# Kernel optimization log

Hardware: AMD Instinct MI355X
Metric: run time of the kernel (lower is better)

## Reference

```python
import jax, jax.numpy as jnp
import numpy as np
import math

N_NODES = 50000
N_EDGES = 400000
D = 256
H = 4
HD = D // H


def _layernorm(x, g, b, eps=1e-5):
    mu = jnp.mean(x, axis=-1, keepdims=True)
    var = jnp.mean((x - mu) ** 2, axis=-1, keepdims=True)
    return (x - mu) * jax.lax.rsqrt(var + eps) * g + b


def setup_inputs() -> dict:
    key = jax.random.key(0)
    ks = jax.random.split(key, 16)
    init = lambda k, sh: (jax.random.normal(k, sh, dtype=jnp.float32) * 0.02)
    inp = {
        "h_n": jax.random.normal(ks[0], (N_NODES, D), dtype=jnp.float32),
        "h_e": jax.random.normal(ks[1], (N_EDGES, D), dtype=jnp.float32),
        "edge_index": jax.random.randint(ks[2], (2, N_EDGES), 0, N_NODES, dtype=jnp.int64),
        "Wq_w": init(ks[3], (2 * D, D)), "Wq_b": jnp.zeros((D,), jnp.float32),
        "Wkv_w": init(ks[4], (2 * D, 2 * D)), "Wkv_b": jnp.zeros((2 * D,), jnp.float32),
        "Wo_w": init(ks[5], (D, D)), "Wo_b": jnp.zeros((D,), jnp.float32),
        "ln1_g": jnp.ones((D,), jnp.float32), "ln1_b": jnp.zeros((D,), jnp.float32),
        "ffn1_w": init(ks[6], (D, 4 * D)), "ffn1_b": jnp.zeros((4 * D,), jnp.float32),
        "ffn2_w": init(ks[7], (4 * D, D)), "ffn2_b": jnp.zeros((D,), jnp.float32),
        "ln2_g": jnp.ones((D,), jnp.float32), "ln2_b": jnp.zeros((D,), jnp.float32),
    }
    return inp


def reference(h_n, h_e, edge_index, Wq_w, Wq_b, Wkv_w, Wkv_b, Wo_w, Wo_b,
              ln1_g, ln1_b, ffn1_w, ffn1_b, ffn2_w, ffn2_b, ln2_g, ln2_b):
    num_nodes = h_n.shape[0]
    src, dst = edge_index[0], edge_index[1]

    # edge gathers
    q_input = jnp.concatenate([h_n[src], h_e], axis=-1)   # (E, 2D)
    kv_input = jnp.concatenate([h_n[dst], h_e], axis=-1)  # (E, 2D)

    Q = q_input @ Wq_w + Wq_b                             # (E, D)
    KV = kv_input @ Wkv_w + Wkv_b                         # (E, 2D)
    K, V = KV[:, :D], KV[:, D:]

    Q = Q.reshape(-1, H, HD)
    K = K.reshape(-1, H, HD)
    V = V.reshape(-1, H, HD)

    scores = jnp.sum(Q * K, axis=-1) / math.sqrt(HD)      # (E, H)

    # scatter softmax over edges grouped by src node
    m = jax.ops.segment_max(scores, src, num_segments=num_nodes)  # (N, H)
    ex = jnp.exp(scores - m[src])
    denom = jax.ops.segment_sum(ex, src, num_segments=num_nodes)  # (N, H)
    attn = ex / denom[src]                                        # (E, H)

    # scatter-sum of weighted values back to src nodes
    wv = attn[:, :, None] * V                                     # (E, H, HD)
    out = jax.ops.segment_sum(wv, src, num_segments=num_nodes)    # (N, H, HD)
    out = out.reshape(num_nodes, D)
    out = out @ Wo_w + Wo_b

    h = _layernorm(h_n + out, ln1_g, ln1_b)
    ff = jax.nn.gelu(h @ ffn1_w + ffn1_b, approximate=False) @ ffn2_w + ffn2_b
    h = _layernorm(h + ff, ln2_g, ln2_b)
    return h
```

## Files before the change

kernel.cpp:

```cpp
#include <hip/hip_runtime.h>
#include <hip/hip_bf16.h>
#include <cstdint>
#include <cstddef>


typedef __bf16 bf16;
typedef bf16 bf16x8 __attribute__((ext_vector_type(8)));
typedef bf16 bf16x4v __attribute__((ext_vector_type(4)));
typedef float f32x4 __attribute__((ext_vector_type(4)));
typedef const uint32_t __attribute__((address_space(1)))* gas_u32p;
typedef uint32_t __attribute__((address_space(3)))* las_u32p;

#define DEV static __device__ __forceinline__

static constexpr int NN = 50000;
static constexpr int NE = 400000;

DEV void async_copy16(const void* g, void* l) {
  __builtin_amdgcn_global_load_lds((gas_u32p)g, (las_u32p)l, 16, 0, 0);
}
DEV float bf2f(bf16 x) { return (float)x; }
DEV bf16  f2bf(float x) { return (bf16)x; }

template <int KT, int EPI>
__global__ __launch_bounds__(256, 2) void gemm_node(
    const bf16* __restrict__ A, int M, const bf16* __restrict__ WT,
    const float* __restrict__ bias, int Nout, float* __restrict__ outf,
    bf16* __restrict__ outb) {
  __shared__ bf16 Al[128 * 32];
  __shared__ bf16 Bl[128 * 32];
  const int tid = threadIdx.x;
  const int n0 = blockIdx.x * 128;
  const int m0 = blockIdx.y * 128;
  const bf16* ab[2];
  const bf16* bb[2];
#pragma unroll
  for (int p = 0; p < 2; ++p) {
    int c = tid + 256 * p;
    int row = c >> 2;
    int c8 = (c & 3) * 8;
    int rg = m0 + row;
    if (rg > M - 1) rg = M - 1;
    ab[p] = A + (size_t)rg * KT + c8;
    bb[p] = WT + (size_t)(n0 + row) * KT + c8;
  }
  const int wv = tid >> 6, lane = tid & 63;
  const int quad = lane >> 4, l16 = lane & 15;
  const int wrow = (wv >> 1) * 64, wcol = (wv & 1) * 64;
  f32x4 acc[4][4] = {};
  for (int k0 = 0; k0 < KT; k0 += 32) {
    if (k0) __syncthreads();
#pragma unroll
    for (int p = 0; p < 2; ++p) {
      async_copy16(ab[p] + k0, &Al[(tid + 256 * p) * 8]);
      async_copy16(bb[p] + k0, &Bl[(tid + 256 * p) * 8]);
    }
    __syncthreads();
    bf16x8 af[4], bfr[4];
#pragma unroll
    for (int t = 0; t < 4; ++t)
      af[t] = *(const bf16x8*)&Al[(wrow + t * 16 + l16) * 32 + quad * 8];
#pragma unroll
    for (int t = 0; t < 4; ++t)
      bfr[t] = *(const bf16x8*)&Bl[(wcol + t * 16 + l16) * 32 + quad * 8];
#pragma unroll
    for (int mt = 0; mt < 4; ++mt)
#pragma unroll
      for (int nt = 0; nt < 4; ++nt)
        acc[mt][nt] = __builtin_amdgcn_mfma_f32_16x16x32_bf16(
            af[mt], bfr[nt], acc[mt][nt], 0, 0, 0);
  }
#pragma unroll
  for (int nt = 0; nt < 4; ++nt) {
    int col = n0 + wcol + nt * 16 + l16;
    float bv = bias ? bias[col] : 0.f;
#pragma unroll
    for (int mt = 0; mt < 4; ++mt)
#pragma unroll
      for (int r = 0; r < 4; ++r) {
        int row = m0 + wrow + mt * 16 + quad * 4 + r;
        if (row < M) {
          float v = acc[mt][nt][r] + bv;
          if (EPI == 0)
            outf[(size_t)row * Nout + col] = v;
          else if (EPI == 1)
            outb[(size_t)row * Nout + col] =
                f2bf(0.5f * v * (1.f + erff(v * 0.70710678118654752f)));
          else
            outb[(size_t)row * Nout + col] = f2bf(v);
        }
      }
  }
}

__global__ __launch_bounds__(256, 2) void gemm_eeq(
    const bf16* __restrict__ he, const bf16* __restrict__ WT,
    const float* __restrict__ bias, const int* __restrict__ src,
    const float* __restrict__ ENf, bf16* __restrict__ Qout) {
  __shared__ bf16 Al[128 * 32];
  __shared__ bf16 Bl[128 * 32];
  const int tid = threadIdx.x;
  const int n0 = blockIdx.x * 128;
  const int m0 = blockIdx.y * 128;
  const bf16* ab[2];
  const bf16* bb[2];
#pragma unroll
  for (int p = 0; p < 2; ++p) {
    int c = tid + 256 * p;
    int row = c >> 2;
    int c8 = (c & 3) * 8;
    ab[p] = he + (size_t)(m0 + row) * 256 + c8;
    bb[p] = WT + (size_t)(n0 + row) * 256 + c8;
  }
  const int wv = tid >> 6, lane = tid & 63;
  const int quad = lane >> 4, l16 = lane & 15;
  const int wrow = (wv >> 1) * 64, wcol = (wv & 1) * 64;
  f32x4 acc[4][4] = {};
  for (int k0 = 0; k0 < 256; k0 += 32) {
    if (k0) __syncthreads();
#pragma unroll
    for (int p = 0; p < 2; ++p) {
      async_copy16(ab[p] + k0, &Al[(tid + 256 * p) * 8]);
      async_copy16(bb[p] + k0, &Bl[(tid + 256 * p) * 8]);
    }
    __syncthreads();
    bf16x8 af[4], bfr[4];
#pragma unroll
    for (int t = 0; t < 4; ++t)
      af[t] = *(const bf16x8*)&Al[(wrow + t * 16 + l16) * 32 + quad * 8];
#pragma unroll
    for (int t = 0; t < 4; ++t)
      bfr[t] = *(const bf16x8*)&Bl[(wcol + t * 16 + l16) * 32 + quad * 8];
#pragma unroll
    for (int mt = 0; mt < 4; ++mt)
#pragma unroll
      for (int nt = 0; nt < 4; ++nt)
        acc[mt][nt] = __builtin_amdgcn_mfma_f32_16x16x32_bf16(
            af[mt], bfr[nt], acc[mt][nt], 0, 0, 0);
  }
  float bv[4];
#pragma unroll
  for (int nt = 0; nt < 4; ++nt) bv[nt] = bias[n0 + wcol + nt * 16 + l16];
#pragma unroll
  for (int mt = 0; mt < 4; ++mt)
#pragma unroll
    for (int r = 0; r < 4; ++r) {
      int row = m0 + wrow + mt * 16 + quad * 4 + r;
      int s = src[row];
      const float* en = ENf + (size_t)s * 512;
#pragma unroll
      for (int nt = 0; nt < 4; ++nt) {
        int col = n0 + wcol + nt * 16 + l16;
        Qout[(size_t)row * 256 + col] = f2bf(acc[mt][nt][r] + bv[nt] + en[col]);
      }
    }
}

__global__ __launch_bounds__(256, 2) void gemm_eek(
    const bf16* __restrict__ he, const bf16* __restrict__ WT,
    const float* __restrict__ bias, const int* __restrict__ dstp,
    const float* __restrict__ ENf, const bf16* __restrict__ Qbf,
    float* __restrict__ scores) {
  __shared__ bf16 Al[128 * 32];
  __shared__ bf16 Bl[128 * 32];
  const int tid = threadIdx.x;
  const int n0 = blockIdx.x * 128;
  const int m0 = blockIdx.y * 128;
  const bf16* ab[2];
  const bf16* bb[2];
#pragma unroll
  for (int p = 0; p < 2; ++p) {
    int c = tid + 256 * p;
    int row = c >> 2;
    int c8 = (c & 3) * 8;
    ab[p] = he + (size_t)(m0 + row) * 256 + c8;
    bb[p] = WT + (size_t)(n0 + row) * 256 + c8;
  }
  const int wv = tid >> 6, lane = tid & 63;
  const int quad = lane >> 4, l16 = lane & 15;
  const int wrow = (wv >> 1) * 64, wcol = (wv & 1) * 64;
  f32x4 acc[4][4] = {};
  for (int k0 = 0; k0 < 256; k0 += 32) {
    if (k0) __syncthreads();
#pragma unroll
    for (int p = 0; p < 2; ++p) {
      async_copy16(ab[p] + k0, &Al[(tid + 256 * p) * 8]);
      async_copy16(bb[p] + k0, &Bl[(tid + 256 * p) * 8]);
    }
    __syncthreads();
    bf16x8 af[4], bfr[4];
#pragma unroll
    for (int t = 0; t < 4; ++t)
      af[t] = *(const bf16x8*)&Al[(wrow + t * 16 + l16) * 32 + quad * 8];
#pragma unroll
    for (int t = 0; t < 4; ++t)
      bfr[t] = *(const bf16x8*)&Bl[(wcol + t * 16 + l16) * 32 + quad * 8];
#pragma unroll
    for (int mt = 0; mt < 4; ++mt)
#pragma unroll
      for (int nt = 0; nt < 4; ++nt)
        acc[mt][nt] = __builtin_amdgcn_mfma_f32_16x16x32_bf16(
            af[mt], bfr[nt], acc[mt][nt], 0, 0, 0);
  }
  float bv[4];
#pragma unroll
  for (int nt = 0; nt < 4; ++nt) bv[nt] = bias[n0 + wcol + nt * 16 + l16];
  const int head = (n0 + wcol) >> 6;
#pragma unroll
  for (int mt = 0; mt < 4; ++mt)
#pragma unroll
    for (int r = 0; r < 4; ++r) {
      int row = m0 + wrow + mt * 16 + quad * 4 + r;
      int d = dstp[row];
      const float* en = ENf + (size_t)d * 512 + 256;
      const bf16* qr = Qbf + (size_t)row * 256;
      float part = 0.f;
#pragma unroll
      for (int nt = 0; nt < 4; ++nt) {
        int col = n0 + wcol + nt * 16 + l16;
        float kv = acc[mt][nt][r] + bv[nt] + en[col];
        part += kv * bf2f(qr[col]);
      }
      part += __shfl_xor(part, 1);
      part += __shfl_xor(part, 2);
      part += __shfl_xor(part, 4);
      part += __shfl_xor(part, 8);
      if (l16 == 0) scores[(size_t)row * 4 + head] = part * 0.125f;
    }
}

__global__ __launch_bounds__(256) void cast_bf16(const float* __restrict__ in,
                                                 bf16* __restrict__ out, int n) {
  int i = (blockIdx.x * 256 + threadIdx.x) * 4;
  if (i < n) {
    float4 v = *(const float4*)(in + i);
    bf16x4v o = {f2bf(v.x), f2bf(v.y), f2bf(v.z), f2bf(v.w)};
    *(bf16x4v*)(out + i) = o;
  }
}

__global__ __launch_bounds__(256) void transpose_cast(
    const float* __restrict__ W, bf16* __restrict__ WT, int K, int N) {
  int i = blockIdx.x * 256 + threadIdx.x;
  if (i < K * N) {
    int k = i / N, n = i - k * N;
    WT[(size_t)n * K + k] = f2bf(W[i]);
  }
}

__global__ __launch_bounds__(256) void build_wnet(
    const float* __restrict__ Wq, const float* __restrict__ Wkv,
    bf16* __restrict__ WnT, bf16* __restrict__ WeT) {
  int n = blockIdx.x, k = threadIdx.x;
  float vn, ve;
  if (n < 256) {
    vn = Wq[(size_t)k * 256 + n];
    ve = Wq[(size_t)(256 + k) * 256 + n];
  } else {
    vn = Wkv[(size_t)k * 512 + (n - 256)];
    ve = Wkv[(size_t)(256 + k) * 512 + (n - 256)];
  }
  WnT[(size_t)n * 256 + k] = f2bf(vn);
  WeT[(size_t)n * 256 + k] = f2bf(ve);
}

__global__ __launch_bounds__(256) void build_wcomb(
    const float* __restrict__ Wkv, const float* __restrict__ Wkv_b,
    const float* __restrict__ Wo, const float* __restrict__ Wo_b,
    bf16* __restrict__ WcombT, float* __restrict__ bias_vo) {
  int j = blockIdx.x, t = threadIdx.x;
  __shared__ float wo[256];
  wo[t] = Wo[(size_t)t * 256 + j];
  __syncthreads();
#pragma unroll
  for (int p = 0; p < 8; ++p) {
    int idx = p * 256 + t;
    int h = idx >> 9, i = idx & 511;
    const float* wrow = Wkv + (size_t)i * 512 + 256 + h * 64;
    const float* wob = wo + h * 64;
    float s = 0.f;
#pragma unroll 8
    for (int m = 0; m < 64; ++m) s += wrow[m] * wob[m];
    WcombT[(size_t)j * 2048 + idx] = f2bf(s);
  }
  float bs = Wkv_b[256 + t] * wo[t];
#pragma unroll
  for (int o = 32; o; o >>= 1) bs += __shfl_xor(bs, o);
  __shared__ float red[4];
  int wv = t >> 6, lane = t & 63;
  if (lane == 0) red[wv] = bs;
  __syncthreads();
  if (t == 0) bias_vo[j] = red[0] + red[1] + red[2] + red[3] + Wo_b[j];
}

__global__ __launch_bounds__(256) void count_deg(const int* __restrict__ src,
                                                 int* __restrict__ deg, int nE) {
  int e = blockIdx.x * 256 + threadIdx.x;
  if (e < nE) atomicAdd(&deg[src[e]], 1);
}

__global__ __launch_bounds__(256) void scan_offs(const int* __restrict__ deg,
                                                 int* __restrict__ offs,
                                                 int* __restrict__ cursor,
                                                 int nN) {
  __shared__ int part[256];
  int tid = threadIdx.x;
  int per = (nN + 255) >> 8;
  int lo = tid * per, hi = lo + per;
  if (hi > nN) hi = nN;
  int sm = 0;
  for (int i = lo; i < hi; ++i) sm += deg[i];
  part[tid] = sm;
  __syncthreads();
  if (tid == 0) {
    int run = 0;
    for (int i = 0; i < 256; ++i) {
      int v = part[i];
      part[i] = run;
      run += v;
    }
  }
  __syncthreads();
  int run = part[tid];
  for (int i = lo; i < hi; ++i) {
    offs[i] = run;
    cursor[i] = run;
    run += deg[i];
  }
  if (tid == 255) offs[nN] = run;
}

__global__ __launch_bounds__(256) void scatter_edges(const int* __restrict__ src,
                                                     int* __restrict__ cursor,
                                                     int* __restrict__ eperm,
                                                     int nE) {
  int e = blockIdx.x * 256 + threadIdx.x;
  if (e < nE) {
    int p = atomicAdd(&cursor[src[e]], 1);
    eperm[p] = e;
  }
}

__global__ __launch_bounds__(256) void aggregate(
    const int* __restrict__ offs, const int* __restrict__ eperm,
    const int* __restrict__ dstp, const float* __restrict__ scores,
    const bf16* __restrict__ hn, const bf16* __restrict__ he,
    bf16* __restrict__ aggH) {
  int n = blockIdx.x;
  int s = offs[n];
  int deg = offs[n + 1] - s;
  int tid = threadIdx.x, wv = tid >> 6, lane = tid & 63;
  __shared__ float mdl[4], dnl[4];
  float mx = -3.4e38f;
  for (int i = lane; i < deg; i += 64) {
    int e = eperm[s + i];
    mx = fmaxf(mx, scores[(size_t)e * 4 + wv]);
  }
#pragma unroll
  for (int o = 32; o; o >>= 1) mx = fmaxf(mx, __shfl_xor(mx, o));
  float sm = 0.f;
  for (int i = lane; i < deg; i += 64) {
    int e = eperm[s + i];
    sm += expf(scores[(size_t)e * 4 + wv] - mx);
  }
#pragma unroll
  for (int o = 32; o; o >>= 1) sm += __shfl_xor(sm, o);
  if (lane == 0) {
    mdl[wv] = mx;
    dnl[wv] = sm;
  }
  __syncthreads();
  float m[4], rd[4];
#pragma unroll
  for (int h = 0; h < 4; ++h) {
    m[h] = mdl[h];
    rd[h] = dnl[h] > 0.f ? 1.f / dnl[h] : 0.f;
  }
  float accn[4] = {}, acce[4] = {};
  for (int i = 0; i < deg; ++i) {
    int e = eperm[s + i];
    int d = dstp[e];
    f32x4 sc = *(const f32x4*)(scores + (size_t)e * 4);
    float w[4];
#pragma unroll
    for (int h = 0; h < 4; ++h) w[h] = expf(sc[h] - m[h]) * rd[h];
    float xn = bf2f(hn[(size_t)d * 256 + tid]);
    float xe = bf2f(he[(size_t)e * 256 + tid]);
#pragma unroll
    for (int h = 0; h < 4; ++h) {
      accn[h] += w[h] * xn;
      acce[h] += w[h] * xe;
    }
  }
  bf16* out = aggH + (size_t)n * 2048;
#pragma unroll
  for (int h = 0; h < 4; ++h) {
    out[h * 512 + tid] = f2bf(accn[h]);
    out[h * 512 + 256 + tid] = f2bf(acce[h]);
  }
}

__global__ __launch_bounds__(256) void ln_kernel(
    const float* __restrict__ x1, const float* __restrict__ x2,
    const float* __restrict__ g, const float* __restrict__ b,
    float* __restrict__ outf, bf16* __restrict__ outb) {
  int n = blockIdx.x, tid = threadIdx.x;
  float x = x1[(size_t)n * 256 + tid] + x2[(size_t)n * 256 + tid];
  float s = x, s2 = x * x;
#pragma unroll
  for (int o = 32; o; o >>= 1) {
    s += __shfl_xor(s, o);
    s2 += __shfl_xor(s2, o);
  }
  __shared__ float ls[4], ls2[4];
  int wv = tid >> 6, lane = tid & 63;
  if (lane == 0) {
    ls[wv] = s;
    ls2[wv] = s2;
  }
  __syncthreads();
  s = ls[0] + ls[1] + ls[2] + ls[3];
  s2 = ls2[0] + ls2[1] + ls2[2] + ls2[3];
  float mu = s * (1.f / 256.f);
  float var = s2 * (1.f / 256.f) - mu * mu;
  float y = (x - mu) * rsqrtf(var + 1e-5f) * g[tid] + b[tid];
  if (outf) outf[(size_t)n * 256 + tid] = y;
  if (outb) outb[(size_t)n * 256 + tid] = f2bf(y);
}

static constexpr size_t OFF_HN    = 0;
static constexpr size_t OFF_HE    = 25600000;
static constexpr size_t OFF_WNT   = 230400000;
static constexpr size_t OFF_WET   = 230662144;
static constexpr size_t OFF_WCT   = 230924288;
static constexpr size_t OFF_W1T   = 231972864;
static constexpr size_t OFF_W2T   = 232497152;
static constexpr size_t OFF_BVO   = 233021440;
static constexpr size_t OFF_SC    = 233022464;
static constexpr size_t OFF_DEG   = 239422464;
static constexpr size_t OFF_OFFS  = 239622464;
static constexpr size_t OFF_CUR   = 239822528;
static constexpr size_t OFF_EPERM = 240022528;
static constexpr size_t OFF_ENF   = 241622528;
static constexpr size_t OFF_Q     = 344022528;
static constexpr size_t OFF_AGGH  = OFF_Q;
static constexpr size_t OFF_TMP   = OFF_HE;
static constexpr size_t OFF_H1F   = OFF_HE + 51200000;
static constexpr size_t OFF_H1B   = OFF_HE + 102400000;
static constexpr size_t OFF_TMP2  = OFF_HE + 128000000;
static constexpr size_t OFF_FFM   = OFF_Q;

extern "C" void kernel_launch(void* const* d_in, const int* in_sizes, int n_in,
                              void* d_out, int out_size, void* d_ws,
                              size_t ws_size, hipStream_t stream) {
  const float* h_n = (const float*)d_in[0];
  const float* h_e = (const float*)d_in[1];
  const int* eidx = (const int*)d_in[2];
  const int* src = eidx;
  const int* dst = eidx + NE;
  const float* Wq_w = (const float*)d_in[3];
  const float* Wq_b = (const float*)d_in[4];
  const float* Wkv_w = (const float*)d_in[5];
  const float* Wkv_b = (const float*)d_in[6];
  const float* Wo_w = (const float*)d_in[7];
  const float* Wo_b = (const float*)d_in[8];
  const float* ln1_g = (const float*)d_in[9];
  const float* ln1_b = (const float*)d_in[10];
  const float* f1_w = (const float*)d_in[11];
  const float* f1_b = (const float*)d_in[12];
  const float* f2_w = (const float*)d_in[13];
  const float* f2_b = (const float*)d_in[14];
  const float* ln2_g = (const float*)d_in[15];
  const float* ln2_b = (const float*)d_in[16];

  uint8_t* ws = (uint8_t*)d_ws;
  bf16* hn_bf = (bf16*)(ws + OFF_HN);
  bf16* he_bf = (bf16*)(ws + OFF_HE);
  bf16* WnT = (bf16*)(ws + OFF_WNT);
  bf16* WeT = (bf16*)(ws + OFF_WET);
  bf16* WcombT = (bf16*)(ws + OFF_WCT);
  bf16* W1T = (bf16*)(ws + OFF_W1T);
  bf16* W2T = (bf16*)(ws + OFF_W2T);
  float* bias_vo = (float*)(ws + OFF_BVO);
  float* scores = (float*)(ws + OFF_SC);
  int* deg = (int*)(ws + OFF_DEG);
  int* offs = (int*)(ws + OFF_OFFS);
  int* cursor = (int*)(ws + OFF_CUR);
  int* eperm = (int*)(ws + OFF_EPERM);
  float* ENf = (float*)(ws + OFF_ENF);
  bf16* Qbf = (bf16*)(ws + OFF_Q);
  bf16* aggH = (bf16*)(ws + OFF_AGGH);
  float* tmp = (float*)(ws + OFF_TMP);
  float* h1f = (float*)(ws + OFF_H1F);
  bf16* h1b = (bf16*)(ws + OFF_H1B);
  float* tmp2 = (float*)(ws + OFF_TMP2);
  bf16* ffm = (bf16*)(ws + OFF_FFM);

  cast_bf16<<<12500, 256, 0, stream>>>(h_n, hn_bf, NN * 256);
  cast_bf16<<<100000, 256, 0, stream>>>(h_e, he_bf, NE * 256);
  build_wnet<<<512, 256, 0, stream>>>(Wq_w, Wkv_w, WnT, WeT);
  build_wcomb<<<256, 256, 0, stream>>>(Wkv_w, Wkv_b, Wo_w, Wo_b, WcombT,
                                       bias_vo);
  transpose_cast<<<1024, 256, 0, stream>>>(f1_w, W1T, 256, 1024);
  transpose_cast<<<1024, 256, 0, stream>>>(f2_w, W2T, 1024, 256);

  hipMemsetAsync(deg, 0, NN * sizeof(int), stream);
  count_deg<<<1563, 256, 0, stream>>>(src, deg, NE);
  scan_offs<<<1, 256, 0, stream>>>(deg, offs, cursor, NN);
  scatter_edges<<<1563, 256, 0, stream>>>(src, cursor, eperm, NE);

  gemm_node<256, 0><<<dim3(4, 391), 256, 0, stream>>>(hn_bf, NN, WnT, nullptr,
                                                      512, ENf, nullptr);
  gemm_eeq<<<dim3(2, 3125), 256, 0, stream>>>(he_bf, WeT, Wq_b, src, ENf, Qbf);
  gemm_eek<<<dim3(2, 3125), 256, 0, stream>>>(he_bf, WeT + 256 * 256, Wkv_b,
                                              dst, ENf, Qbf, scores);

  aggregate<<<NN, 256, 0, stream>>>(offs, eperm, dst, scores, hn_bf, he_bf,
                                    aggH);

  gemm_node<2048, 0><<<dim3(2, 391), 256, 0, stream>>>(aggH, NN, WcombT,
                                                       bias_vo, 256, tmp,
                                                       nullptr);
  ln_kernel<<<NN, 256, 0, stream>>>(h_n, tmp, ln1_g, ln1_b, h1f, h1b);

  gemm_node<256, 1><<<dim3(8, 391), 256, 0, stream>>>(h1b, NN, W1T, f1_b, 1024,
                                                      nullptr, ffm);
  gemm_node<1024, 0><<<dim3(2, 391), 256, 0, stream>>>(ffm, NN, W2T, f2_b, 256,
                                                       tmp2, nullptr);
  ln_kernel<<<NN, 256, 0, stream>>>(h1f, tmp2, ln2_g, ln2_b, (float*)d_out,
                                    nullptr);
}
```

Before: 1.896 ms.

## Fuse Q/K edge GEMMs and sort edge data by source node

Merges the separate Q and K edge GEMMs into one kernel that computes both accumulators from a shared A tile and forms attention scores directly. This removes the bf16 Q round-trip through global memory and one pass over h_e. Edge features, src and dst are permuted into src-sorted order during the bf16 cast, so the aggregate kernel reads edges contiguously instead of through eperm. The aggregate kernel also precomputes softmax weights per 64-edge chunk in shared memory. In exchange the fused GEMM holds twice the accumulators, which raises register pressure, and the cast now does a gathered read.

```diff
diff --git a/kernel.cpp b/kernel.cpp
--- a/kernel.cpp
+++ b/kernel.cpp
@@ -83,143 +83,93 @@
           float v = acc[mt][nt][r] + bv;
           if (EPI == 0)
             outf[(size_t)row * Nout + col] = v;
-          else if (EPI == 1)
+          else
             outb[(size_t)row * Nout + col] =
                 f2bf(0.5f * v * (1.f + erff(v * 0.70710678118654752f)));
-          else
-            outb[(size_t)row * Nout + col] = f2bf(v);
         }
       }
   }
 }
 
-__global__ __launch_bounds__(256, 2) void gemm_eeq(
-    const bf16* __restrict__ he, const bf16* __restrict__ WT,
-    const float* __restrict__ bias, const int* __restrict__ src,
-    const float* __restrict__ ENf, bf16* __restrict__ Qout) {
+__global__ __launch_bounds__(256, 2) void gemm_qk(
+    const bf16* __restrict__ he, const bf16* __restrict__ WTq,
+    const bf16* __restrict__ WTk, const float* __restrict__ bq,
+    const float* __restrict__ bk, const int* __restrict__ sp,
+    const int* __restrict__ dp, const float* __restrict__ ENf,
+    float* __restrict__ scores) {
   __shared__ bf16 Al[128 * 32];
-  __shared__ bf16 Bl[128 * 32];
+  __shared__ bf16 Bq[128 * 32];
+  __shared__ bf16 Bk[128 * 32];
   const int tid = threadIdx.x;
   const int n0 = blockIdx.x * 128;
   const int m0 = blockIdx.y * 128;
   const bf16* ab[2];
-  const bf16* bb[2];
+  const bf16* bqp[2];
+  const bf16* bkp[2];
 #pragma unroll
   for (int p = 0; p < 2; ++p) {
     int c = tid + 256 * p;
     int row = c >> 2;
     int c8 = (c & 3) * 8;
     ab[p] = he + (size_t)(m0 + row) * 256 + c8;
-    bb[p] = WT + (size_t)(n0 + row) * 256 + c8;
+    bqp[p] = WTq + (size_t)(n0 + row) * 256 + c8;
+    bkp[p] = WTk + (size_t)(n0 + row) * 256 + c8;
   }
   const int wv = tid >> 6, lane = tid & 63;
   const int quad = lane >> 4, l16 = lane & 15;
   const int wrow = (wv >> 1) * 64, wcol = (wv & 1) * 64;
-  f32x4 acc[4][4] = {};
+  f32x4 aq[4][4] = {};
+  f32x4 ak[4][4] = {};
   for (int k0 = 0; k0 < 256; k0 += 32) {
     if (k0) __syncthreads();
 #pragma unroll
     for (int p = 0; p < 2; ++p) {
       async_copy16(ab[p] + k0, &Al[(tid + 256 * p) * 8]);
-      async_copy16(bb[p] + k0, &Bl[(tid + 256 * p) * 8]);
+      async_copy16(bqp[p] + k0, &Bq[(tid + 256 * p) * 8]);
+      async_copy16(bkp[p] + k0, &Bk[(tid + 256 * p) * 8]);
     }
     __syncthreads();
-    bf16x8 af[4], bfr[4];
+    bf16x8 af[4];
 #pragma unroll
     for (int t = 0; t < 4; ++t)
       af[t] = *(const bf16x8*)&Al[(wrow + t * 16 + l16) * 32 + quad * 8];
 #pragma unroll
-    for (int t = 0; t < 4; ++t)
-      bfr[t] = *(const bf16x8*)&Bl[(wcol + t * 16 + l16) * 32 + quad * 8];
-#pragma unroll
-    for (int mt = 0; mt < 4; ++mt)
-#pragma unroll
-      for (int nt = 0; nt < 4; ++nt)
-        acc[mt][nt] = __builtin_amdgcn_mfma_f32_16x16x32_bf16(
-            af[mt], bfr[nt], acc[mt][nt], 0, 0, 0);
-  }
-  float bv[4];
-#pragma unroll
-  for (int nt = 0; nt < 4; ++nt) bv[nt] = bias[n0 + wcol + nt * 16 + l16];
+    for (int nt = 0; nt < 4; ++nt) {
+      bf16x8 fq = *(const bf16x8*)&Bq[(wcol + nt * 16 + l16) * 32 + quad * 8];
+#pragma unroll
+      for (int mt = 0; mt < 4; ++mt)
+        aq[mt][nt] = __builtin_amdgcn_mfma_f32_16x16x32_bf16(af[mt], fq,
+                                                             aq[mt][nt], 0, 0, 0);
+      bf16x8 fk = *(const bf16x8*)&Bk[(wcol + nt * 16 + l16) * 32 + quad * 8];
+#pragma unroll
+      for (int mt = 0; mt < 4; ++mt)
+        ak[mt][nt] = __builtin_amdgcn_mfma_f32_16x16x32_bf16(af[mt], fk,
+                                                             ak[mt][nt], 0, 0, 0);
+    }
+  }
+  float bvq[4], bvk[4];
+#pragma unroll
+  for (int nt = 0; nt < 4; ++nt) {
+    int col = n0 + wcol + nt * 16 + l16;
+    bvq[nt] = bq[col];
+    bvk[nt] = bk[col];
+  }
+  const int head = (n0 + wcol) >> 6;
 #pragma unroll
   for (int mt = 0; mt < 4; ++mt)
 #pragma unroll
     for (int r = 0; r < 4; ++r) {
       int row = m0 + wrow + mt * 16 + quad * 4 + r;
-      int s = src[row];
-      const float* en = ENf + (size_t)s * 512;
+      int s_ = sp[row], d_ = dp[row];
+      const float* eq = ENf + (size_t)s_ * 512;
+      const float* ek = ENf + (size_t)d_ * 512 + 256;
+      float part = 0.f;
 #pragma unroll
       for (int nt = 0; nt < 4; ++nt) {
         int col = n0 + wcol + nt * 16 + l16;
-        Qout[(size_t)row * 256 + col] = f2bf(acc[mt][nt][r] + bv[nt] + en[col]);
-      }
-    }
-}
-
-__global__ __launch_bounds__(256, 2) void gemm_eek(
-    const bf16* __restrict__ he, const bf16* __restrict__ WT,
-    const float* __restrict__ bias, const int* __restrict__ dstp,
-    const float* __restrict__ ENf, const bf16* __restrict__ Qbf,
-    float* __restrict__ scores) {
-  __shared__ bf16 Al[128 * 32];
-  __shared__ bf16 Bl[128 * 32];
-  const int tid = threadIdx.x;
-  const int n0 = blockIdx.x * 128;
-  const int m0 = blockIdx.y * 128;
-  const bf16* ab[2];
-  const bf16* bb[2];
-#pragma unroll
-  for (int p = 0; p < 2; ++p) {
-    int c = tid + 256 * p;
-    int row = c >> 2;
-    int c8 = (c & 3) * 8;
-    ab[p] = he + (size_t)(m0 + row) * 256 + c8;
-    bb[p] = WT + (size_t)(n0 + row) * 256 + c8;
-  }
-  const int wv = tid >> 6, lane = tid & 63;
-  const int quad = lane >> 4, l16 = lane & 15;
-  const int wrow = (wv >> 1) * 64, wcol = (wv & 1) * 64;
-  f32x4 acc[4][4] = {};
-  for (int k0 = 0; k0 < 256; k0 += 32) {
-    if (k0) __syncthreads();
-#pragma unroll
-    for (int p = 0; p < 2; ++p) {
-      async_copy16(ab[p] + k0, &Al[(tid + 256 * p) * 8]);
-      async_copy16(bb[p] + k0, &Bl[(tid + 256 * p) * 8]);
-    }
-    __syncthreads();
-    bf16x8 af[4], bfr[4];
-#pragma unroll
-    for (int t = 0; t < 4; ++t)
-      af[t] = *(const bf16x8*)&Al[(wrow + t * 16 + l16) * 32 + quad * 8];
-#pragma unroll
-    for (int t = 0; t < 4; ++t)
-      bfr[t] = *(const bf16x8*)&Bl[(wcol + t * 16 + l16) * 32 + quad * 8];
-#pragma unroll
-    for (int mt = 0; mt < 4; ++mt)
-#pragma unroll
-      for (int nt = 0; nt < 4; ++nt)
-        acc[mt][nt] = __builtin_amdgcn_mfma_f32_16x16x32_bf16(
-            af[mt], bfr[nt], acc[mt][nt], 0, 0, 0);
-  }
-  float bv[4];
-#pragma unroll
-  for (int nt = 0; nt < 4; ++nt) bv[nt] = bias[n0 + wcol + nt * 16 + l16];
-  const int head = (n0 + wcol) >> 6;
-#pragma unroll
-  for (int mt = 0; mt < 4; ++mt)
-#pragma unroll
-    for (int r = 0; r < 4; ++r) {
-      int row = m0 + wrow + mt * 16 + quad * 4 + r;
-      int d = dstp[row];
-      const float* en = ENf + (size_t)d * 512 + 256;
-      const bf16* qr = Qbf + (size_t)row * 256;
-      float part = 0.f;
-#pragma unroll
-      for (int nt = 0; nt < 4; ++nt) {
-        int col = n0 + wcol + nt * 16 + l16;
-        float kv = acc[mt][nt][r] + bv[nt] + en[col];
-        part += kv * bf2f(qr[col]);
+        float qv = aq[mt][nt][r] + bvq[nt] + eq[col];
+        float kv = ak[mt][nt][r] + bvk[nt] + ek[col];
+        part += qv * kv;
       }
       part += __shfl_xor(part, 1);
       part += __shfl_xor(part, 2);
@@ -236,6 +186,30 @@
     float4 v = *(const float4*)(in + i);
     bf16x4v o = {f2bf(v.x), f2bf(v.y), f2bf(v.z), f2bf(v.w)};
     *(bf16x4v*)(out + i) = o;
+  }
+}
+
+__global__ __launch_bounds__(256) void cast_he_perm(
+    const float* __restrict__ in, const int* __restrict__ eperm,
+    bf16* __restrict__ out) {
+  int p = blockIdx.x * 4 + (threadIdx.x >> 6);
+  int c4 = (threadIdx.x & 63) * 4;
+  int e = eperm[p];
+  float4 v = *(const float4*)(in + (size_t)e * 256 + c4);
+  bf16x4v o = {f2bf(v.x), f2bf(v.y), f2bf(v.z), f2bf(v.w)};
+  *(bf16x4v*)(out + (size_t)p * 256 + c4) = o;
+}
+
+__global__ __launch_bounds__(256) void perm_sd(const int* __restrict__ src,
+                                               const int* __restrict__ dst,
+                                               const int* __restrict__ eperm,
+                                               int* __restrict__ sp,
+                                               int* __restrict__ dp, int nE) {
+  int p = blockIdx.x * 256 + threadIdx.x;
+  if (p < nE) {
+    int e = eperm[p];
+    sp[p] = src[e];
+    dp[p] = dst[e];
   }
 }
 
@@ -342,27 +316,23 @@
 }
 
 __global__ __launch_bounds__(256) void aggregate(
-    const int* __restrict__ offs, const int* __restrict__ eperm,
-    const int* __restrict__ dstp, const float* __restrict__ scores,
-    const bf16* __restrict__ hn, const bf16* __restrict__ he,
-    bf16* __restrict__ aggH) {
+    const int* __restrict__ offs, const int* __restrict__ dp,
+    const float* __restrict__ scores, const bf16* __restrict__ hn,
+    const bf16* __restrict__ he, bf16* __restrict__ aggH) {
   int n = blockIdx.x;
   int s = offs[n];
   int deg = offs[n + 1] - s;
   int tid = threadIdx.x, wv = tid >> 6, lane = tid & 63;
   __shared__ float mdl[4], dnl[4];
+  __shared__ float wl[64][4];
   float mx = -3.4e38f;
-  for (int i = lane; i < deg; i += 64) {
-    int e = eperm[s + i];
-    mx = fmaxf(mx, scores[(size_t)e * 4 + wv]);
-  }
+  for (int i = lane; i < deg; i += 64)
+    mx = fmaxf(mx, scores[(size_t)(s + i) * 4 + wv]);
 #pragma unroll
   for (int o = 32; o; o >>= 1) mx = fmaxf(mx, __shfl_xor(mx, o));
   float sm = 0.f;
-  for (int i = lane; i < deg; i += 64) {
-    int e = eperm[s + i];
-    sm += expf(scores[(size_t)e * 4 + wv] - mx);
-  }
+  for (int i = lane; i < deg; i += 64)
+    sm += expf(scores[(size_t)(s + i) * 4 + wv] - mx);
 #pragma unroll
   for (int o = 32; o; o >>= 1) sm += __shfl_xor(sm, o);
   if (lane == 0) {
@@ -370,27 +340,29 @@
     dnl[wv] = sm;
   }
   __syncthreads();
-  float m[4], rd[4];
-#pragma unroll
-  for (int h = 0; h < 4; ++h) {
-    m[h] = mdl[h];
-    rd[h] = dnl[h] > 0.f ? 1.f / dnl[h] : 0.f;
-  }
+  const float mh = mdl[wv];
+  const float rdh = dnl[wv] > 0.f ? 1.f / dnl[wv] : 0.f;
   float accn[4] = {}, acce[4] = {};
-  for (int i = 0; i < deg; ++i) {
-    int e = eperm[s + i];
-    int d = dstp[e];
-    f32x4 sc = *(const f32x4*)(scores + (size_t)e * 4);
-    float w[4];
-#pragma unroll
-    for (int h = 0; h < 4; ++h) w[h] = expf(sc[h] - m[h]) * rd[h];
-    float xn = bf2f(hn[(size_t)d * 256 + tid]);
-    float xe = bf2f(he[(size_t)e * 256 + tid]);
-#pragma unroll
-    for (int h = 0; h < 4; ++h) {
-      accn[h] += w[h] * xn;
-      acce[h] += w[h] * xe;
-    }
+  for (int c0 = 0; c0 < deg; c0 += 64) {
+    int nc = deg - c0;
+    if (nc > 64) nc = 64;
+    if (lane < nc) {
+      float sc = scores[(size_t)(s + c0 + lane) * 4 + wv];
+      wl[lane][wv] = expf(sc - mh) * rdh;
+    }
+    __syncthreads();
+    for (int i = 0; i < nc; ++i) {
+      size_t p = (size_t)(s + c0 + i);
+      int d = dp[p];
+      float4 w4 = *(const float4*)wl[i];
+      float xn = bf2f(hn[(size_t)d * 256 + tid]);
+      float xe = bf2f(he[p * 256 + tid]);
+      accn[0] += w4.x * xn; acce[0] += w4.x * xe;
+      accn[1] += w4.y * xn; acce[1] += w4.y * xe;
+      accn[2] += w4.z * xn; acce[2] += w4.z * xe;
+      accn[3] += w4.w * xn; acce[3] += w4.w * xe;
+    }
+    __syncthreads();
   }
   bf16* out = aggH + (size_t)n * 2048;
 #pragma unroll
@@ -441,14 +413,15 @@
 static constexpr size_t OFF_OFFS  = 239622464;
 static constexpr size_t OFF_CUR   = 239822528;
 static constexpr size_t OFF_EPERM = 240022528;
-static constexpr size_t OFF_ENF   = 241622528;
-static constexpr size_t OFF_Q     = 344022528;
-static constexpr size_t OFF_AGGH  = OFF_Q;
+static constexpr size_t OFF_SP    = 241622528;
+static constexpr size_t OFF_DP    = 243222528;
+static constexpr size_t OFF_ENF   = 244822528;
+static constexpr size_t OFF_AGGH  = 347222528;
 static constexpr size_t OFF_TMP   = OFF_HE;
 static constexpr size_t OFF_H1F   = OFF_HE + 51200000;
 static constexpr size_t OFF_H1B   = OFF_HE + 102400000;
 static constexpr size_t OFF_TMP2  = OFF_HE + 128000000;
-static constexpr size_t OFF_FFM   = OFF_Q;
+static constexpr size_t OFF_FFM   = OFF_AGGH;
 
 extern "C" void kernel_launch(void* const* d_in, const int* in_sizes, int n_in,
                               void* d_out, int out_size, void* d_ws,
@@ -487,8 +460,9 @@
   int* offs = (int*)(ws + OFF_OFFS);
   int* cursor = (int*)(ws + OFF_CUR);
   int* eperm = (int*)(ws + OFF_EPERM);
+  int* sp = (int*)(ws + OFF_SP);
+  int* dp = (int*)(ws + OFF_DP);
   float* ENf = (float*)(ws + OFF_ENF);
-  bf16* Qbf = (bf16*)(ws + OFF_Q);
   bf16* aggH = (bf16*)(ws + OFF_AGGH);
   float* tmp = (float*)(ws + OFF_TMP);
   float* h1f = (float*)(ws + OFF_H1F);
@@ -497,7 +471,6 @@
   bf16* ffm = (bf16*)(ws + OFF_FFM);
 
   cast_bf16<<<12500, 256, 0, stream>>>(h_n, hn_bf, NN * 256);
-  cast_bf16<<<100000, 256, 0, stream>>>(h_e, he_bf, NE * 256);
   build_wnet<<<512, 256, 0, stream>>>(Wq_w, Wkv_w, WnT, WeT);
   build_wcomb<<<256, 256, 0, stream>>>(Wkv_w, Wkv_b, Wo_w, Wo_b, WcombT,
                                        bias_vo);
@@ -508,15 +481,15 @@
   count_deg<<<1563, 256, 0, stream>>>(src, deg, NE);
   scan_offs<<<1, 256, 0, stream>>>(deg, offs, cursor, NN);
   scatter_edges<<<1563, 256, 0, stream>>>(src, cursor, eperm, NE);
+  perm_sd<<<1563, 256, 0, stream>>>(src, dst, eperm, sp, dp, NE);
+  cast_he_perm<<<100000, 256, 0, stream>>>(h_e, eperm, he_bf);
 
   gemm_node<256, 0><<<dim3(4, 391), 256, 0, stream>>>(hn_bf, NN, WnT, nullptr,
                                                       512, ENf, nullptr);
-  gemm_eeq<<<dim3(2, 3125), 256, 0, stream>>>(he_bf, WeT, Wq_b, src, ENf, Qbf);
-  gemm_eek<<<dim3(2, 3125), 256, 0, stream>>>(he_bf, WeT + 256 * 256, Wkv_b,
-                                              dst, ENf, Qbf, scores);
-
-  aggregate<<<NN, 256, 0, stream>>>(offs, eperm, dst, scores, hn_bf, he_bf,
-                                    aggH);
+  gemm_qk<<<dim3(2, 3125), 256, 0, stream>>>(he_bf, WeT, WeT + 256 * 256, Wq_b,
+                                             Wkv_b, sp, dp, ENf, scores);
+
+  aggregate<<<NN, 256, 0, stream>>>(offs, dp, scores, hn_bf, he_bf, aggH);
 
   gemm_node<2048, 0><<<dim3(2, 391), 256, 0, stream>>>(aggH, NN, WcombT,
                                                        bias_vo, 256, tmp,
```

After: 1.697 ms. 1.12x faster.
